# Kernel optimization log

Hardware: AMD Instinct MI355X
Metric: run time of the kernel (lower is better)

## Reference

```python
import jax, jax.numpy as jnp
import numpy as np
from jax import lax

EPS = 1e-5


def _conv1d(x, w, groups=1):
    # x: [B, Cin, L], w: [Cout, Cin/groups, K], padding=1, stride=1
    return lax.conv_general_dilated(
        x, w, window_strides=(1,), padding=[(1, 1)],
        dimension_numbers=('NCH', 'OIH', 'NCH'),
        feature_group_count=groups)


def _batchnorm(x, gamma, beta):
    # training-mode BatchNorm1d: stats over (batch, length), biased variance
    mean = jnp.mean(x, axis=(0, 2), keepdims=True)
    var = jnp.mean(jnp.square(x - mean), axis=(0, 2), keepdims=True)
    xn = (x - mean) * lax.rsqrt(var + EPS)
    return xn * gamma[None, :, None] + beta[None, :, None]


def setup_inputs() -> dict:
    key = jax.random.key(0)
    ks = jax.random.split(key, 8)
    B = 1 << 20  # 1,048,576
    x = jax.random.normal(ks[0], (B, 3), dtype=jnp.float32)
    # conv1: 1 -> 16, k=3 (xavier-normal-ish scale)
    w1 = jax.random.normal(ks[1], (16, 1, 3), dtype=jnp.float32) * 0.5
    b1 = jnp.zeros((16,), jnp.float32)
    g1 = jnp.ones((16,), jnp.float32)
    bt1 = jnp.zeros((16,), jnp.float32)
    # conv2: grouped, groups=16, 16 -> 32, k=3 -> weight [32, 1, 3]
    w2 = jax.random.normal(ks[2], (32, 1, 3), dtype=jnp.float32) * 0.5
    b2 = jnp.zeros((32,), jnp.float32)
    g2 = jnp.ones((32,), jnp.float32)
    bt2 = jnp.zeros((32,), jnp.float32)
    # fc1: Linear(32 -> 16) kaiming-normal-ish
    fw1 = jax.random.normal(ks[3], (16, 32), dtype=jnp.float32) * (2.0 / 32.0) ** 0.5
    fb1 = jnp.zeros((16,), jnp.float32)
    # fc2: Linear(16 -> 1); torch init sets these to 0, but use small random
    # values so gradients/outputs are non-degenerate for testing
    fw2 = jax.random.normal(ks[4], (1, 16), dtype=jnp.float32) * 0.1
    fb2 = jnp.zeros((1,), jnp.float32)
    return dict(x=x, w1=w1, b1=b1, g1=g1, bt1=bt1,
                w2=w2, b2=b2, g2=g2, bt2=bt2,
                fw1=fw1, fb1=fb1, fw2=fw2, fb2=fb2)


def reference(x, w1, b1, g1, bt1, w2, b2, g2, bt2, fw1, fb1, fw2, fb2):
    h = x[:, None, :]                                   # [B, 1, 3]
    h = _conv1d(h, w1) + b1[None, :, None]              # [B, 16, 3]
    h = _batchnorm(jax.nn.relu(h), g1, bt1)
    h = _conv1d(h, w2, groups=16) + b2[None, :, None]   # [B, 32, 3]
    h = _batchnorm(jax.nn.relu(h), g2, bt2)
    h = jnp.mean(h, axis=2)                             # AdaptiveAvgPool1d(1) -> [B, 32]
    h = jax.nn.relu(h @ fw1.T + fb1)                    # [B, 16]
    return h @ fw2.T + fb2                              # [B, 1]
```

## Files before the change

### kernel.cpp

```cpp
#include <hip/hip_runtime.h>
#include <math.h>

#define EPSV 1e-5f

__device__ __forceinline__ void conv3_relu(float x0, float x1, float x2,
                                           float wa, float wb, float wc, float bb,
                                           float& t0, float& t1, float& t2)
{
    t0 = fmaxf(fmaf(wb, x0, fmaf(wc, x1, bb)), 0.f);
    t1 = fmaxf(fmaf(wa, x0, fmaf(wb, x1, fmaf(wc, x2, bb))), 0.f);
    t2 = fmaxf(fmaf(wa, x1, fmaf(wb, x2, bb)), 0.f);
}

__global__ __launch_bounds__(256) void k_stats1(const float* __restrict__ x,
                                                const float* __restrict__ w1,
                                                const float* __restrict__ b1,
                                                float* __restrict__ partials,
                                                int B)
{
    __shared__ float4 sW1[16];
    int t = threadIdx.x;
    if (t < 16) sW1[t] = make_float4(w1[3*t], w1[3*t+1], w1[3*t+2], b1[t]);
    __syncthreads();

    float cur[32];
#pragma unroll
    for (int i = 0; i < 32; ++i) cur[i] = 0.f;

    auto upd = [&](int g, float t0, float t1, float t2) {
        cur[g]      += t0 + t1 + t2;
        cur[16 + g]  = fmaf(t0, t0, fmaf(t1, t1, fmaf(t2, t2, cur[16 + g])));
    };

    auto accum1 = [&](float x0, float x1, float x2) {
#pragma unroll
        for (int g = 0; g < 16; ++g) {
            float4 w = sW1[g];
            float t0, t1, t2;
            conv3_relu(x0, x1, x2, w.x, w.y, w.z, w.w, t0, t1, t2);
            upd(g, t0, t1, t2);
        }
    };

    int nchunk = (B + 3) >> 2;
    for (int ch = blockIdx.x * 256 + t; ch < nchunk; ch += gridDim.x * 256) {
        int s0 = ch << 2;
        if (s0 + 4 <= B) {
            const float4* xp = (const float4*)(x + (size_t)s0 * 3);
            float4 A = xp[0], Bq = xp[1], Cq = xp[2];
            const float xs[4][3] = {{A.x,  A.y,  A.z },
                                    {A.w,  Bq.x, Bq.y},
                                    {Bq.z, Bq.w, Cq.x},
                                    {Cq.y, Cq.z, Cq.w}};
#pragma unroll
            for (int g = 0; g < 16; ++g) {
                float4 w = sW1[g];
#pragma unroll
                for (int m = 0; m < 4; ++m) {
                    float t0, t1, t2;
                    conv3_relu(xs[m][0], xs[m][1], xs[m][2],
                               w.x, w.y, w.z, w.w, t0, t1, t2);
                    upd(g, t0, t1, t2);
                }
            }
        } else {
            for (int m = 0; m < 4; ++m) {
                int s = s0 + m;
                if (s < B) accum1(x[3*s], x[3*s+1], x[3*s+2]);
            }
        }
    }

    int lane = t & 63, wid = t >> 6;
#pragma unroll
    for (int i = 0; i < 32; ++i) cur[i] += __shfl_xor(cur[i], 32, 64);
#pragma unroll
    for (int half = 16; half >= 1; half >>= 1) {
#pragma unroll
        for (int i = 0; i < half; ++i) {
            bool up = (lane & half);
            float keep = up ? cur[i + half] : cur[i];
            float send = up ? cur[i] : cur[i + half];
            cur[i] = keep + __shfl_xor(send, half, 64);
        }
    }
    __shared__ float red[4][32];
    if (lane < 32) red[wid][lane] = cur[0];
    __syncthreads();
    if (t < 32)
        partials[blockIdx.x * 32 + t] = red[0][t] + red[1][t] + red[2][t] + red[3][t];
}

__global__ __launch_bounds__(256) void k_stats2(const float* __restrict__ x,
                                                const float* __restrict__ w1,
                                                const float* __restrict__ b1,
                                                const float* __restrict__ p1,
                                                const float* __restrict__ g1,
                                                const float* __restrict__ bt1,
                                                const float* __restrict__ w2,
                                                const float* __restrict__ b2,
                                                float* __restrict__ partials,
                                                float Ninv, int nb1, int B)
{
    __shared__ float4 sW1[16];
    __shared__ float4 sU[32];
    __shared__ float2 sC[32];
    __shared__ float4 redbuf[256];
    __shared__ float tot[32];
    __shared__ float ssc[16], ssh[16];
    int t = threadIdx.x;

    {
        int v4 = t & 7, c = t >> 3;
        float4 a = make_float4(0.f, 0.f, 0.f, 0.f);
        for (int b = c; b < nb1; b += 32) {
            float4 p = ((const float4*)p1)[b * 8 + v4];
            a.x += p.x; a.y += p.y; a.z += p.z; a.w += p.w;
        }
        redbuf[c * 8 + v4] = a;
    }
    if (t < 16) sW1[t] = make_float4(w1[3*t], w1[3*t+1], w1[3*t+2], b1[t]);
    __syncthreads();
    if (t < 8) {
        float4 a = make_float4(0.f, 0.f, 0.f, 0.f);
#pragma unroll
        for (int c = 0; c < 32; ++c) {
            float4 p = redbuf[c * 8 + t];
            a.x += p.x; a.y += p.y; a.z += p.z; a.w += p.w;
        }
        tot[4*t+0] = a.x; tot[4*t+1] = a.y; tot[4*t+2] = a.z; tot[4*t+3] = a.w;
    }
    __syncthreads();
    if (t < 16) {
        float mean = tot[t] * Ninv;
        float var  = fmaxf(tot[16 + t] * Ninv - mean * mean, 0.f);
        float rstd = rsqrtf(var + EPSV);
        float sc = g1[t] * rstd;
        ssc[t] = sc;
        ssh[t] = bt1[t] - mean * sc;
    }
    __syncthreads();
    if (t < 32) {
        int o = t, g = o >> 1;
        float sc = ssc[g], sh = ssh[g];
        float wv0 = w2[3*o], wv1 = w2[3*o+1], wv2 = w2[3*o+2];
        sU[o] = make_float4(wv0 * sc, wv1 * sc, wv2 * sc,
                            b2[o] + sh * (wv1 + wv2));
        sC[o] = make_float2(b2[o] + sh * (wv0 + wv1 + wv2),
                            b2[o] + sh * (wv0 + wv1));
    }
    __syncthreads();

    const int p = t & 1;
    const int gbase = 8 * p;

    float cur[32];
#pragma unroll
    for (int i = 0; i < 32; ++i) cur[i] = 0.f;

    auto updc = [&](int oc, float v0, float v1, float v2) {
        cur[oc]      += v0 + v1 + v2;
        cur[16 + oc]  = fmaf(v0, v0, fmaf(v1, v1, fmaf(v2, v2, cur[16 + oc])));
    };

    auto accum4 = [&](const float4& A, const float4& Bq, const float4& Cq) {
        const float xs[4][3] = {{A.x,  A.y,  A.z },
                                {A.w,  Bq.x, Bq.y},
                                {Bq.z, Bq.w, Cq.x},
                                {Cq.y, Cq.z, Cq.w}};
#pragma unroll
        for (int g = 0; g < 8; ++g) {
            float4 w = sW1[gbase + g];
            float r[4][3];
#pragma unroll
            for (int m = 0; m < 4; ++m)
                conv3_relu(xs[m][0], xs[m][1], xs[m][2],
                           w.x, w.y, w.z, w.w, r[m][0], r[m][1], r[m][2]);
#pragma unroll
            for (int jj = 0; jj < 2; ++jj) {
                int oc = 2 * g + jj;
                int oo = 16 * p + oc;
                float4 u = sU[oo];
                float2 cc = sC[oo];
#pragma unroll
                for (int m = 0; m < 4; ++m) {
                    float v0 = fmaxf(fmaf(u.y, r[m][0], fmaf(u.z, r[m][1], u.w)), 0.f);
                    float v1 = fmaxf(fmaf(u.x, r[m][0], fmaf(u.y, r[m][1], fmaf(u.z, r[m][2], cc.x))), 0.f);
                    float v2 = fmaxf(fmaf(u.x, r[m][1], fmaf(u.y, r[m][2], cc.y)), 0.f);
                    updc(oc, v0, v1, v2);
                }
            }
        }
    };

    auto accum1 = [&](float x0, float x1, float x2) {
#pragma unroll
        for (int g = 0; g < 8; ++g) {
            float4 w = sW1[gbase + g];
            float r0, r1, r2;
            conv3_relu(x0, x1, x2, w.x, w.y, w.z, w.w, r0, r1, r2);
#pragma unroll
            for (int jj = 0; jj < 2; ++jj) {
                int oc = 2 * g + jj;
                int oo = 16 * p + oc;
                float4 u = sU[oo];
                float2 cc = sC[oo];
                float v0 = fmaxf(fmaf(u.y, r0, fmaf(u.z, r1, u.w)), 0.f);
                float v1 = fmaxf(fmaf(u.x, r0, fmaf(u.y, r1, fmaf(u.z, r2, cc.x))), 0.f);
                float v2 = fmaxf(fmaf(u.x, r1, fmaf(u.y, r2, cc.y)), 0.f);
                updc(oc, v0, v1, v2);
            }
        }
    };

    int nchunk = (B + 3) >> 2;
    int gp     = (blockIdx.x * 256 + t) >> 1;
    int stride = (gridDim.x * 256) >> 1;
    for (int ch = gp; ch < nchunk; ch += stride) {
        int s0 = ch << 2;
        if (s0 + 4 <= B) {
            const float4* xp = (const float4*)(x + (size_t)s0 * 3);
            float4 A = xp[0], Bq = xp[1], Cq = xp[2];
            accum4(A, Bq, Cq);
        } else {
            for (int m = 0; m < 4; ++m) {
                int s = s0 + m;
                if (s < B) accum1(x[3*s], x[3*s+1], x[3*s+2]);
            }
        }
    }

    int lane = t & 63, wid = t >> 6;
#pragma unroll
    for (int half = 16; half >= 1; half >>= 1) {
        int d = half << 1;
#pragma unroll
        for (int i = 0; i < half; ++i) {
            bool up = (lane & d);
            float keep = up ? cur[i + half] : cur[i];
            float send = up ? cur[i] : cur[i + half];
            cur[i] = keep + __shfl_xor(send, d, 64);
        }
    }
    __shared__ float red[4][64];
    {
        int idx = lane >> 1;
        int v = ((idx >> 4) << 5) + 16 * p + (idx & 15);
        red[wid][v] = cur[0];
    }
    __syncthreads();
    if (t < 64)
        partials[blockIdx.x * 64 + t] = red[0][t] + red[1][t] + red[2][t] + red[3][t];
}

__global__ __launch_bounds__(256, 2) void k_final(const float* __restrict__ x,
                                                  const float* __restrict__ w1,
                                                  const float* __restrict__ b1,
                                                  const float* __restrict__ w2,
                                                  const float* __restrict__ b2,
                                                  const float* __restrict__ g1,
                                                  const float* __restrict__ bt1,
                                                  const float* __restrict__ g2,
                                                  const float* __restrict__ bt2,
                                                  const float* __restrict__ fw1,
                                                  const float* __restrict__ fb1,
                                                  const float* __restrict__ fw2,
                                                  const float* __restrict__ fb2,
                                                  const float* __restrict__ p1,
                                                  const float* __restrict__ p2,
                                                  float* __restrict__ out,
                                                  float Ninv, int nb1, int nb2, int B)
{
    __shared__ float4 sW1[16];
    __shared__ float4 sU[32];
    __shared__ float2 sC[32];
    __shared__ float4 sFT[128];
    __shared__ float2 sJ[16];
    __shared__ float  sb2;
    __shared__ float4 redbuf[256];
    __shared__ float tot1[32];
    __shared__ float tot2[64];
    __shared__ float ssc1[16], ssh1[16];
    __shared__ float ssc2[32], ssh2[32];
    int t = threadIdx.x;

    {
        int v4 = t & 7, c = t >> 3;
        float4 a = make_float4(0.f, 0.f, 0.f, 0.f);
        for (int b = c; b < nb1; b += 32) {
            float4 p = ((const float4*)p1)[b * 8 + v4];
            a.x += p.x; a.y += p.y; a.z += p.z; a.w += p.w;
        }
        redbuf[c * 8 + v4] = a;
    }
    if (t < 16) sW1[t] = make_float4(w1[3*t], w1[3*t+1], w1[3*t+2], b1[t]);
    if (t == 224) sb2 = fb2[0];
    __syncthreads();
    if (t < 8) {
        float4 a = make_float4(0.f, 0.f, 0.f, 0.f);
#pragma unroll
        for (int c = 0; c < 32; ++c) {
            float4 p = redbuf[c * 8 + t];
            a.x += p.x; a.y += p.y; a.z += p.z; a.w += p.w;
        }
        tot1[4*t+0] = a.x; tot1[4*t+1] = a.y; tot1[4*t+2] = a.z; tot1[4*t+3] = a.w;
    }
    __syncthreads();
    if (t < 16) {
        float mean = tot1[t] * Ninv;
        float var  = fmaxf(tot1[16 + t] * Ninv - mean * mean, 0.f);
        float rstd = rsqrtf(var + EPSV);
        float sc = g1[t] * rstd;
        ssc1[t] = sc;
        ssh1[t] = bt1[t] - mean * sc;
    }
    __syncthreads();
    if (t < 32) {
        int o = t, g = o >> 1;
        float sc = ssc1[g], sh = ssh1[g];
        float wv0 = w2[3*o], wv1 = w2[3*o+1], wv2 = w2[3*o+2];
        sU[o] = make_float4(wv0 * sc, wv1 * sc, wv2 * sc,
                            b2[o] + sh * (wv1 + wv2));
        sC[o] = make_float2(b2[o] + sh * (wv0 + wv1 + wv2),
                            b2[o] + sh * (wv0 + wv1));
    }
    {
        int v4 = t & 15, c = t >> 4;
        float4 a = make_float4(0.f, 0.f, 0.f, 0.f);
        for (int b = c; b < nb2; b += 16) {
            float4 p = ((const float4*)p2)[b * 16 + v4];
            a.x += p.x; a.y += p.y; a.z += p.z; a.w += p.w;
        }
        redbuf[c * 16 + v4] = a;
    }
    __syncthreads();
    if (t < 16) {
        float4 a = make_float4(0.f, 0.f, 0.f, 0.f);
#pragma unroll
        for (int c = 0; c < 16; ++c) {
            float4 p = redbuf[c * 16 + t];
            a.x += p.x; a.y += p.y; a.z += p.z; a.w += p.w;
        }
        tot2[4*t+0] = a.x; tot2[4*t+1] = a.y; tot2[4*t+2] = a.z; tot2[4*t+3] = a.w;
    }
    __syncthreads();
    if (t < 32) {
        float mean = tot2[t] * Ninv;
        float var  = fmaxf(tot2[32 + t] * Ninv - mean * mean, 0.f);
        float rstd = rsqrtf(var + EPSV);
        float sc = g2[t] * rstd;
        ssc2[t] = sc;
        ssh2[t] = bt2[t] - mean * sc;
    }
    __syncthreads();
    for (int idx = t; idx < 512; idx += 256) {
        int o = idx >> 4, j = idx & 15;
        ((float*)sFT)[o * 16 + j] = fw1[j * 32 + o] * ssc2[o] * (1.0f / 3.0f);
    }
    if (t < 16) {
        float a = fb1[t];
#pragma unroll
        for (int c = 0; c < 32; ++c) a = fmaf(fw1[t * 32 + c], ssh2[c], a);
        sJ[t] = make_float2(a, fw2[t]);
    }
    __syncthreads();

    int nchunk = (B + 3) >> 2;
    for (int ch = blockIdx.x * 256 + t; ch < nchunk; ch += gridDim.x * 256) {
        int s0 = ch << 2;
        if (s0 + 4 <= B) {
            const float4* xp = (const float4*)(x + (size_t)s0 * 3);
            float4 A = xp[0], Bq = xp[1], Cq = xp[2];
            const float xs[4][3] = {{A.x,  A.y,  A.z },
                                    {A.w,  Bq.x, Bq.y},
                                    {Bq.z, Bq.w, Cq.x},
                                    {Cq.y, Cq.z, Cq.w}};

            float acc[4][16];
#pragma unroll
            for (int m = 0; m < 4; ++m)
#pragma unroll
                for (int j = 0; j < 16; ++j) acc[m][j] = 0.f;

#pragma unroll 4
            for (int g = 0; g < 16; ++g) {
                float4 w = sW1[g];
                float r[4][3];
#pragma unroll
                for (int m = 0; m < 4; ++m)
                    conv3_relu(xs[m][0], xs[m][1], xs[m][2],
                               w.x, w.y, w.z, w.w, r[m][0], r[m][1], r[m][2]);
#pragma unroll
                for (int jj = 0; jj < 2; ++jj) {
                    int o = 2 * g + jj;
                    float4 u = sU[o];
                    float2 cc = sC[o];
                    float so[4];
#pragma unroll
                    for (int m = 0; m < 4; ++m) {
                        float v0 = fmaxf(fmaf(u.y, r[m][0], fmaf(u.z, r[m][1], u.w)), 0.f);
                        float v1 = fmaxf(fmaf(u.x, r[m][0], fmaf(u.y, r[m][1], fmaf(u.z, r[m][2], cc.x))), 0.f);
                        float v2 = fmaxf(fmaf(u.x, r[m][1], fmaf(u.y, r[m][2], cc.y)), 0.f);
                        so[m] = v0 + v1 + v2;
                    }
#pragma unroll
                    for (int k = 0; k < 4; ++k) {
                        float4 f = sFT[o * 4 + k];
#pragma unroll
                        for (int m = 0; m < 4; ++m) {
                            acc[m][4*k+0] = fmaf(f.x, so[m], acc[m][4*k+0]);
                            acc[m][4*k+1] = fmaf(f.y, so[m], acc[m][4*k+1]);
                            acc[m][4*k+2] = fmaf(f.z, so[m], acc[m][4*k+2]);
                            acc[m][4*k+3] = fmaf(f.w, so[m], acc[m][4*k+3]);
                        }
                    }
                }
            }

            float res[4];
#pragma unroll
            for (int m = 0; m < 4; ++m) res[m] = sb2;
#pragma unroll
            for (int j = 0; j < 16; ++j) {
                float2 jw = sJ[j];
#pragma unroll
                for (int m = 0; m < 4; ++m)
                    res[m] = fmaf(jw.y, fmaxf(acc[m][j] + jw.x, 0.f), res[m]);
            }
            *(float4*)(out + s0) = make_float4(res[0], res[1], res[2], res[3]);
        } else {
            for (int m = 0; m < 4; ++m) {
                int s = s0 + m;
                if (s >= B) break;
                float x0 = x[3*s], x1 = x[3*s+1], x2 = x[3*s+2];
                float acc1[16];
#pragma unroll
                for (int j = 0; j < 16; ++j) acc1[j] = 0.f;
#pragma unroll 4
                for (int g = 0; g < 16; ++g) {
                    float4 w = sW1[g];
                    float r0, r1, r2;
                    conv3_relu(x0, x1, x2, w.x, w.y, w.z, w.w, r0, r1, r2);
#pragma unroll
                    for (int jj = 0; jj < 2; ++jj) {
                        int o = 2 * g + jj;
                        float4 u = sU[o];
                        float2 cc = sC[o];
                        float v0 = fmaxf(fmaf(u.y, r0, fmaf(u.z, r1, u.w)), 0.f);
                        float v1 = fmaxf(fmaf(u.x, r0, fmaf(u.y, r1, fmaf(u.z, r2, cc.x))), 0.f);
                        float v2 = fmaxf(fmaf(u.x, r1, fmaf(u.y, r2, cc.y)), 0.f);
                        float so = v0 + v1 + v2;
#pragma unroll
                        for (int k = 0; k < 4; ++k) {
                            float4 f = sFT[o * 4 + k];
                            acc1[4*k+0] = fmaf(f.x, so, acc1[4*k+0]);
                            acc1[4*k+1] = fmaf(f.y, so, acc1[4*k+1]);
                            acc1[4*k+2] = fmaf(f.z, so, acc1[4*k+2]);
                            acc1[4*k+3] = fmaf(f.w, so, acc1[4*k+3]);
                        }
                    }
                }
                float r = sb2;
#pragma unroll
                for (int j = 0; j < 16; ++j) {
                    float2 jw = sJ[j];
                    r = fmaf(jw.y, fmaxf(acc1[j] + jw.x, 0.f), r);
                }
                out[s] = r;
            }
        }
    }
}

extern "C" void kernel_launch(void* const* d_in, const int* in_sizes, int n_in,
                              void* d_out, int out_size, void* d_ws, size_t ws_size,
                              hipStream_t stream)
{
    const float* x   = (const float*)d_in[0];
    const float* w1  = (const float*)d_in[1];
    const float* b1  = (const float*)d_in[2];
    const float* g1  = (const float*)d_in[3];
    const float* bt1 = (const float*)d_in[4];
    const float* w2  = (const float*)d_in[5];
    const float* b2  = (const float*)d_in[6];
    const float* g2  = (const float*)d_in[7];
    const float* bt2 = (const float*)d_in[8];
    const float* fw1 = (const float*)d_in[9];
    const float* fb1 = (const float*)d_in[10];
    const float* fw2 = (const float*)d_in[11];
    const float* fb2 = (const float*)d_in[12];

    int B = in_sizes[0] / 3;

    int nb1 = 512;
    int nb2 = 512;
    while ((size_t)(nb1 * 32 + nb2 * 64) * sizeof(float) > ws_size && nb1 > 1) {
        nb1 >>= 1; nb2 >>= 1;
    }

    float* ws = (float*)d_ws;
    float* p1 = ws;
    float* p2 = ws + (size_t)nb1 * 32;

    float Ninv = 1.0f / (3.0f * (float)B);

    int nchunk = (B + 3) / 4;
    int gridF = (nchunk + 255) / 256;
    if (gridF > 2048) gridF = 2048;

    k_stats1<<<nb1, 256, 0, stream>>>(x, w1, b1, p1, B);
    k_stats2<<<nb2, 256, 0, stream>>>(x, w1, b1, p1, g1, bt1, w2, b2,
                                      p2, Ninv, nb1, B);
    k_final<<<gridF, 256, 0, stream>>>(x, w1, b1, w2, b2, g1, bt1, g2, bt2,
                                       fw1, fb1, fw2, fb2, p1, p2,
                                       (float*)d_out, Ninv, nb1, nb2, B);
}
```

Baseline: 164.5 us.

## Fuse three passes into one persistent kernel with software grid barriers

Replaces the three separate kernels (stats1, stats2, final) with one persistent kernel. It runs the three phases in sequence, separated by atomic-counter grid barriers, and sizes the grid from occupancy capped at 512 blocks. The aim is to remove kernel launch gaps and to let each block reuse its shared-memory setup. In exchange the final phase runs on at most 512 blocks instead of up to 2048, and every barrier adds spin-wait latency. The barrier relies on all blocks being co-resident and adds a memset launch per call.

```diff
diff --git a/kernel.cpp b/kernel.cpp
--- a/kernel.cpp
+++ b/kernel.cpp
@@ -12,264 +12,41 @@
     t2 = fmaxf(fmaf(wa, x1, fmaf(wb, x2, bb)), 0.f);
 }
 
-__global__ __launch_bounds__(256) void k_stats1(const float* __restrict__ x,
-                                                const float* __restrict__ w1,
-                                                const float* __restrict__ b1,
-                                                float* __restrict__ partials,
-                                                int B)
+__device__ __forceinline__ void grid_barrier(int* count, int* gen, int nb)
 {
-    __shared__ float4 sW1[16];
-    int t = threadIdx.x;
-    if (t < 16) sW1[t] = make_float4(w1[3*t], w1[3*t+1], w1[3*t+2], b1[t]);
     __syncthreads();
-
-    float cur[32];
-#pragma unroll
-    for (int i = 0; i < 32; ++i) cur[i] = 0.f;
-
-    auto upd = [&](int g, float t0, float t1, float t2) {
-        cur[g]      += t0 + t1 + t2;
-        cur[16 + g]  = fmaf(t0, t0, fmaf(t1, t1, fmaf(t2, t2, cur[16 + g])));
-    };
-
-    auto accum1 = [&](float x0, float x1, float x2) {
-#pragma unroll
-        for (int g = 0; g < 16; ++g) {
-            float4 w = sW1[g];
-            float t0, t1, t2;
-            conv3_relu(x0, x1, x2, w.x, w.y, w.z, w.w, t0, t1, t2);
-            upd(g, t0, t1, t2);
-        }
-    };
-
-    int nchunk = (B + 3) >> 2;
-    for (int ch = blockIdx.x * 256 + t; ch < nchunk; ch += gridDim.x * 256) {
-        int s0 = ch << 2;
-        if (s0 + 4 <= B) {
-            const float4* xp = (const float4*)(x + (size_t)s0 * 3);
-            float4 A = xp[0], Bq = xp[1], Cq = xp[2];
-            const float xs[4][3] = {{A.x,  A.y,  A.z },
-                                    {A.w,  Bq.x, Bq.y},
-                                    {Bq.z, Bq.w, Cq.x},
-                                    {Cq.y, Cq.z, Cq.w}};
-#pragma unroll
-            for (int g = 0; g < 16; ++g) {
-                float4 w = sW1[g];
-#pragma unroll
-                for (int m = 0; m < 4; ++m) {
-                    float t0, t1, t2;
-                    conv3_relu(xs[m][0], xs[m][1], xs[m][2],
-                               w.x, w.y, w.z, w.w, t0, t1, t2);
-                    upd(g, t0, t1, t2);
-                }
-            }
+    if (threadIdx.x == 0) {
+        __threadfence();
+        int g = atomicAdd(gen, 0);
+        if (atomicAdd(count, 1) == nb - 1) {
+            atomicExch(count, 0);
+            atomicAdd(gen, 1);
         } else {
-            for (int m = 0; m < 4; ++m) {
-                int s = s0 + m;
-                if (s < B) accum1(x[3*s], x[3*s+1], x[3*s+2]);
-            }
-        }
-    }
-
-    int lane = t & 63, wid = t >> 6;
-#pragma unroll
-    for (int i = 0; i < 32; ++i) cur[i] += __shfl_xor(cur[i], 32, 64);
-#pragma unroll
-    for (int half = 16; half >= 1; half >>= 1) {
-#pragma unroll
-        for (int i = 0; i < half; ++i) {
-            bool up = (lane & half);
-            float keep = up ? cur[i + half] : cur[i];
-            float send = up ? cur[i] : cur[i + half];
-            cur[i] = keep + __shfl_xor(send, half, 64);
-        }
-    }
-    __shared__ float red[4][32];
-    if (lane < 32) red[wid][lane] = cur[0];
-    __syncthreads();
-    if (t < 32)
-        partials[blockIdx.x * 32 + t] = red[0][t] + red[1][t] + red[2][t] + red[3][t];
-}
-
-__global__ __launch_bounds__(256) void k_stats2(const float* __restrict__ x,
-                                                const float* __restrict__ w1,
-                                                const float* __restrict__ b1,
-                                                const float* __restrict__ p1,
-                                                const float* __restrict__ g1,
-                                                const float* __restrict__ bt1,
-                                                const float* __restrict__ w2,
-                                                const float* __restrict__ b2,
-                                                float* __restrict__ partials,
-                                                float Ninv, int nb1, int B)
-{
-    __shared__ float4 sW1[16];
-    __shared__ float4 sU[32];
-    __shared__ float2 sC[32];
-    __shared__ float4 redbuf[256];
-    __shared__ float tot[32];
-    __shared__ float ssc[16], ssh[16];
-    int t = threadIdx.x;
-
-    {
-        int v4 = t & 7, c = t >> 3;
-        float4 a = make_float4(0.f, 0.f, 0.f, 0.f);
-        for (int b = c; b < nb1; b += 32) {
-            float4 p = ((const float4*)p1)[b * 8 + v4];
-            a.x += p.x; a.y += p.y; a.z += p.z; a.w += p.w;
-        }
-        redbuf[c * 8 + v4] = a;
-    }
-    if (t < 16) sW1[t] = make_float4(w1[3*t], w1[3*t+1], w1[3*t+2], b1[t]);
-    __syncthreads();
-    if (t < 8) {
-        float4 a = make_float4(0.f, 0.f, 0.f, 0.f);
-#pragma unroll
-        for (int c = 0; c < 32; ++c) {
-            float4 p = redbuf[c * 8 + t];
-            a.x += p.x; a.y += p.y; a.z += p.z; a.w += p.w;
-        }
-        tot[4*t+0] = a.x; tot[4*t+1] = a.y; tot[4*t+2] = a.z; tot[4*t+3] = a.w;
+            while (atomicAdd(gen, 0) == g) __builtin_amdgcn_s_sleep(2);
+        }
+        __threadfence();
     }
     __syncthreads();
-    if (t < 16) {
-        float mean = tot[t] * Ninv;
-        float var  = fmaxf(tot[16 + t] * Ninv - mean * mean, 0.f);
-        float rstd = rsqrtf(var + EPSV);
-        float sc = g1[t] * rstd;
-        ssc[t] = sc;
-        ssh[t] = bt1[t] - mean * sc;
-    }
-    __syncthreads();
-    if (t < 32) {
-        int o = t, g = o >> 1;
-        float sc = ssc[g], sh = ssh[g];
-        float wv0 = w2[3*o], wv1 = w2[3*o+1], wv2 = w2[3*o+2];
-        sU[o] = make_float4(wv0 * sc, wv1 * sc, wv2 * sc,
-                            b2[o] + sh * (wv1 + wv2));
-        sC[o] = make_float2(b2[o] + sh * (wv0 + wv1 + wv2),
-                            b2[o] + sh * (wv0 + wv1));
-    }
-    __syncthreads();
-
-    const int p = t & 1;
-    const int gbase = 8 * p;
-
-    float cur[32];
-#pragma unroll
-    for (int i = 0; i < 32; ++i) cur[i] = 0.f;
-
-    auto updc = [&](int oc, float v0, float v1, float v2) {
-        cur[oc]      += v0 + v1 + v2;
-        cur[16 + oc]  = fmaf(v0, v0, fmaf(v1, v1, fmaf(v2, v2, cur[16 + oc])));
-    };
-
-    auto accum4 = [&](const float4& A, const float4& Bq, const float4& Cq) {
-        const float xs[4][3] = {{A.x,  A.y,  A.z },
-                                {A.w,  Bq.x, Bq.y},
-                                {Bq.z, Bq.w, Cq.x},
-                                {Cq.y, Cq.z, Cq.w}};
-#pragma unroll
-        for (int g = 0; g < 8; ++g) {
-            float4 w = sW1[gbase + g];
-            float r[4][3];
-#pragma unroll
-            for (int m = 0; m < 4; ++m)
-                conv3_relu(xs[m][0], xs[m][1], xs[m][2],
-                           w.x, w.y, w.z, w.w, r[m][0], r[m][1], r[m][2]);
-#pragma unroll
-            for (int jj = 0; jj < 2; ++jj) {
-                int oc = 2 * g + jj;
-                int oo = 16 * p + oc;
-                float4 u = sU[oo];
-                float2 cc = sC[oo];
-#pragma unroll
-                for (int m = 0; m < 4; ++m) {
-                    float v0 = fmaxf(fmaf(u.y, r[m][0], fmaf(u.z, r[m][1], u.w)), 0.f);
-                    float v1 = fmaxf(fmaf(u.x, r[m][0], fmaf(u.y, r[m][1], fmaf(u.z, r[m][2], cc.x))), 0.f);
-                    float v2 = fmaxf(fmaf(u.x, r[m][1], fmaf(u.y, r[m][2], cc.y)), 0.f);
-                    updc(oc, v0, v1, v2);
-                }
-            }
-        }
-    };
-
-    auto accum1 = [&](float x0, float x1, float x2) {
-#pragma unroll
-        for (int g = 0; g < 8; ++g) {
-            float4 w = sW1[gbase + g];
-            float r0, r1, r2;
-            conv3_relu(x0, x1, x2, w.x, w.y, w.z, w.w, r0, r1, r2);
-#pragma unroll
-            for (int jj = 0; jj < 2; ++jj) {
-                int oc = 2 * g + jj;
-                int oo = 16 * p + oc;
-                float4 u = sU[oo];
-                float2 cc = sC[oo];
-                float v0 = fmaxf(fmaf(u.y, r0, fmaf(u.z, r1, u.w)), 0.f);
-                float v1 = fmaxf(fmaf(u.x, r0, fmaf(u.y, r1, fmaf(u.z, r2, cc.x))), 0.f);
-                float v2 = fmaxf(fmaf(u.x, r1, fmaf(u.y, r2, cc.y)), 0.f);
-                updc(oc, v0, v1, v2);
-            }
-        }
-    };
-
-    int nchunk = (B + 3) >> 2;
-    int gp     = (blockIdx.x * 256 + t) >> 1;
-    int stride = (gridDim.x * 256) >> 1;
-    for (int ch = gp; ch < nchunk; ch += stride) {
-        int s0 = ch << 2;
-        if (s0 + 4 <= B) {
-            const float4* xp = (const float4*)(x + (size_t)s0 * 3);
-            float4 A = xp[0], Bq = xp[1], Cq = xp[2];
-            accum4(A, Bq, Cq);
-        } else {
-            for (int m = 0; m < 4; ++m) {
-                int s = s0 + m;
-                if (s < B) accum1(x[3*s], x[3*s+1], x[3*s+2]);
-            }
-        }
-    }
-
-    int lane = t & 63, wid = t >> 6;
-#pragma unroll
-    for (int half = 16; half >= 1; half >>= 1) {
-        int d = half << 1;
-#pragma unroll
-        for (int i = 0; i < half; ++i) {
-            bool up = (lane & d);
-            float keep = up ? cur[i + half] : cur[i];
-            float send = up ? cur[i] : cur[i + half];
-            cur[i] = keep + __shfl_xor(send, d, 64);
-        }
-    }
-    __shared__ float red[4][64];
-    {
-        int idx = lane >> 1;
-        int v = ((idx >> 4) << 5) + 16 * p + (idx & 15);
-        red[wid][v] = cur[0];
-    }
-    __syncthreads();
-    if (t < 64)
-        partials[blockIdx.x * 64 + t] = red[0][t] + red[1][t] + red[2][t] + red[3][t];
 }
 
-__global__ __launch_bounds__(256, 2) void k_final(const float* __restrict__ x,
-                                                  const float* __restrict__ w1,
-                                                  const float* __restrict__ b1,
-                                                  const float* __restrict__ w2,
-                                                  const float* __restrict__ b2,
-                                                  const float* __restrict__ g1,
-                                                  const float* __restrict__ bt1,
-                                                  const float* __restrict__ g2,
-                                                  const float* __restrict__ bt2,
-                                                  const float* __restrict__ fw1,
-                                                  const float* __restrict__ fb1,
-                                                  const float* __restrict__ fw2,
-                                                  const float* __restrict__ fb2,
-                                                  const float* __restrict__ p1,
-                                                  const float* __restrict__ p2,
-                                                  float* __restrict__ out,
-                                                  float Ninv, int nb1, int nb2, int B)
+__global__ __launch_bounds__(256) void k_fused(const float* __restrict__ x,
+                                               const float* __restrict__ w1,
+                                               const float* __restrict__ b1,
+                                               const float* __restrict__ g1,
+                                               const float* __restrict__ bt1,
+                                               const float* __restrict__ w2,
+                                               const float* __restrict__ b2,
+                                               const float* __restrict__ g2,
+                                               const float* __restrict__ bt2,
+                                               const float* __restrict__ fw1,
+                                               const float* __restrict__ fb1,
+                                               const float* __restrict__ fw2,
+                                               const float* __restrict__ fb2,
+                                               float* __restrict__ p1,
+                                               float* __restrict__ p2,
+                                               int* __restrict__ bar,
+                                               float* __restrict__ out,
+                                               float Ninv, int B)
 {
     __shared__ float4 sW1[16];
     __shared__ float4 sU[32];
@@ -278,113 +55,146 @@
     __shared__ float2 sJ[16];
     __shared__ float  sb2;
     __shared__ float4 redbuf[256];
-    __shared__ float tot1[32];
-    __shared__ float tot2[64];
-    __shared__ float ssc1[16], ssh1[16];
-    __shared__ float ssc2[32], ssh2[32];
+    __shared__ float  tot[64];
+    __shared__ float  ssc[32], ssh[32];
+    __shared__ float  sRed[4][64];
+
     int t = threadIdx.x;
+    int nchunk = (B + 3) >> 2;
+    int NBg = gridDim.x;
 
     {
-        int v4 = t & 7, c = t >> 3;
-        float4 a = make_float4(0.f, 0.f, 0.f, 0.f);
-        for (int b = c; b < nb1; b += 32) {
-            float4 p = ((const float4*)p1)[b * 8 + v4];
-            a.x += p.x; a.y += p.y; a.z += p.z; a.w += p.w;
-        }
-        redbuf[c * 8 + v4] = a;
+        if (t < 16) sW1[t] = make_float4(w1[3*t], w1[3*t+1], w1[3*t+2], b1[t]);
+        __syncthreads();
+
+        float cur[32];
+#pragma unroll
+        for (int i = 0; i < 32; ++i) cur[i] = 0.f;
+
+        auto upd = [&](int g, float t0, float t1, float t2) {
+            cur[g]      += t0 + t1 + t2;
+            cur[16 + g]  = fmaf(t0, t0, fmaf(t1, t1, fmaf(t2, t2, cur[16 + g])));
+        };
+
+        auto accum1 = [&](float x0, float x1, float x2) {
+#pragma unroll
+            for (int g = 0; g < 16; ++g) {
+                float4 w = sW1[g];
+                float t0, t1, t2;
+                conv3_relu(x0, x1, x2, w.x, w.y, w.z, w.w, t0, t1, t2);
+                upd(g, t0, t1, t2);
+            }
+        };
+
+        for (int ch = blockIdx.x * 256 + t; ch < nchunk; ch += NBg * 256) {
+            int s0 = ch << 2;
+            if (s0 + 4 <= B) {
+                const float4* xp = (const float4*)(x + (size_t)s0 * 3);
+                float4 A = xp[0], Bq = xp[1], Cq = xp[2];
+                const float xs[4][3] = {{A.x,  A.y,  A.z },
+                                        {A.w,  Bq.x, Bq.y},
+                                        {Bq.z, Bq.w, Cq.x},
+                                        {Cq.y, Cq.z, Cq.w}};
+#pragma unroll
+                for (int g = 0; g < 16; ++g) {
+                    float4 w = sW1[g];
+#pragma unroll
+                    for (int m = 0; m < 4; ++m) {
+                        float t0, t1, t2;
+                        conv3_relu(xs[m][0], xs[m][1], xs[m][2],
+                                   w.x, w.y, w.z, w.w, t0, t1, t2);
+                        upd(g, t0, t1, t2);
+                    }
+                }
+            } else {
+                for (int m = 0; m < 4; ++m) {
+                    int s = s0 + m;
+                    if (s < B) accum1(x[3*s], x[3*s+1], x[3*s+2]);
+                }
+            }
+        }
+
+        int lane = t & 63, wid = t >> 6;
+#pragma unroll
+        for (int i = 0; i < 32; ++i) cur[i] += __shfl_xor(cur[i], 32, 64);
+#pragma unroll
+        for (int half = 16; half >= 1; half >>= 1) {
+#pragma unroll
+            for (int i = 0; i < half; ++i) {
+                bool up = (lane & half);
+                float keep = up ? cur[i + half] : cur[i];
+                float send = up ? cur[i] : cur[i + half];
+                cur[i] = keep + __shfl_xor(send, half, 64);
+            }
+        }
+        if (lane < 32) sRed[wid][lane] = cur[0];
+        __syncthreads();
+        if (t < 32)
+            p1[blockIdx.x * 32 + t] = sRed[0][t] + sRed[1][t] + sRed[2][t] + sRed[3][t];
     }
-    if (t < 16) sW1[t] = make_float4(w1[3*t], w1[3*t+1], w1[3*t+2], b1[t]);
-    if (t == 224) sb2 = fb2[0];
-    __syncthreads();
-    if (t < 8) {
-        float4 a = make_float4(0.f, 0.f, 0.f, 0.f);
-#pragma unroll
-        for (int c = 0; c < 32; ++c) {
-            float4 p = redbuf[c * 8 + t];
-            a.x += p.x; a.y += p.y; a.z += p.z; a.w += p.w;
-        }
-        tot1[4*t+0] = a.x; tot1[4*t+1] = a.y; tot1[4*t+2] = a.z; tot1[4*t+3] = a.w;
-    }
-    __syncthreads();
-    if (t < 16) {
-        float mean = tot1[t] * Ninv;
-        float var  = fmaxf(tot1[16 + t] * Ninv - mean * mean, 0.f);
-        float rstd = rsqrtf(var + EPSV);
-        float sc = g1[t] * rstd;
-        ssc1[t] = sc;
-        ssh1[t] = bt1[t] - mean * sc;
-    }
-    __syncthreads();
-    if (t < 32) {
-        int o = t, g = o >> 1;
-        float sc = ssc1[g], sh = ssh1[g];
-        float wv0 = w2[3*o], wv1 = w2[3*o+1], wv2 = w2[3*o+2];
-        sU[o] = make_float4(wv0 * sc, wv1 * sc, wv2 * sc,
-                            b2[o] + sh * (wv1 + wv2));
-        sC[o] = make_float2(b2[o] + sh * (wv0 + wv1 + wv2),
-                            b2[o] + sh * (wv0 + wv1));
-    }
+    grid_barrier(bar, bar + 1, NBg);
+
     {
-        int v4 = t & 15, c = t >> 4;
-        float4 a = make_float4(0.f, 0.f, 0.f, 0.f);
-        for (int b = c; b < nb2; b += 16) {
-            float4 p = ((const float4*)p2)[b * 16 + v4];
-            a.x += p.x; a.y += p.y; a.z += p.z; a.w += p.w;
-        }
-        redbuf[c * 16 + v4] = a;
-    }
-    __syncthreads();
-    if (t < 16) {
-        float4 a = make_float4(0.f, 0.f, 0.f, 0.f);
-#pragma unroll
-        for (int c = 0; c < 16; ++c) {
-            float4 p = redbuf[c * 16 + t];
-            a.x += p.x; a.y += p.y; a.z += p.z; a.w += p.w;
-        }
-        tot2[4*t+0] = a.x; tot2[4*t+1] = a.y; tot2[4*t+2] = a.z; tot2[4*t+3] = a.w;
-    }
-    __syncthreads();
-    if (t < 32) {
-        float mean = tot2[t] * Ninv;
-        float var  = fmaxf(tot2[32 + t] * Ninv - mean * mean, 0.f);
-        float rstd = rsqrtf(var + EPSV);
-        float sc = g2[t] * rstd;
-        ssc2[t] = sc;
-        ssh2[t] = bt2[t] - mean * sc;
-    }
-    __syncthreads();
-    for (int idx = t; idx < 512; idx += 256) {
-        int o = idx >> 4, j = idx & 15;
-        ((float*)sFT)[o * 16 + j] = fw1[j * 32 + o] * ssc2[o] * (1.0f / 3.0f);
-    }
-    if (t < 16) {
-        float a = fb1[t];
-#pragma unroll
-        for (int c = 0; c < 32; ++c) a = fmaf(fw1[t * 32 + c], ssh2[c], a);
-        sJ[t] = make_float2(a, fw2[t]);
-    }
-    __syncthreads();
-
-    int nchunk = (B + 3) >> 2;
-    for (int ch = blockIdx.x * 256 + t; ch < nchunk; ch += gridDim.x * 256) {
-        int s0 = ch << 2;
-        if (s0 + 4 <= B) {
-            const float4* xp = (const float4*)(x + (size_t)s0 * 3);
-            float4 A = xp[0], Bq = xp[1], Cq = xp[2];
+        {
+            int v4 = t & 7, c = t >> 3;
+            float4 a = make_float4(0.f, 0.f, 0.f, 0.f);
+            for (int b = c; b < NBg; b += 32) {
+                float4 p = ((const float4*)p1)[b * 8 + v4];
+                a.x += p.x; a.y += p.y; a.z += p.z; a.w += p.w;
+            }
+            redbuf[c * 8 + v4] = a;
+        }
+        __syncthreads();
+        if (t < 8) {
+            float4 a = make_float4(0.f, 0.f, 0.f, 0.f);
+#pragma unroll
+            for (int c = 0; c < 32; ++c) {
+                float4 p = redbuf[c * 8 + t];
+                a.x += p.x; a.y += p.y; a.z += p.z; a.w += p.w;
+            }
+            tot[4*t+0] = a.x; tot[4*t+1] = a.y; tot[4*t+2] = a.z; tot[4*t+3] = a.w;
+        }
+        __syncthreads();
+        if (t < 16) {
+            float mean = tot[t] * Ninv;
+            float var  = fmaxf(tot[16 + t] * Ninv - mean * mean, 0.f);
+            float rstd = rsqrtf(var + EPSV);
+            float sc = g1[t] * rstd;
+            ssc[t] = sc;
+            ssh[t] = bt1[t] - mean * sc;
+        }
+        __syncthreads();
+        if (t < 32) {
+            int o = t, g = o >> 1;
+            float sc = ssc[g], sh = ssh[g];
+            float wv0 = w2[3*o], wv1 = w2[3*o+1], wv2 = w2[3*o+2];
+            sU[o] = make_float4(wv0 * sc, wv1 * sc, wv2 * sc,
+                                b2[o] + sh * (wv1 + wv2));
+            sC[o] = make_float2(b2[o] + sh * (wv0 + wv1 + wv2),
+                                b2[o] + sh * (wv0 + wv1));
+        }
+        __syncthreads();
+
+        const int p = t & 1;
+        const int gbase = 8 * p;
+
+        float cur[32];
+#pragma unroll
+        for (int i = 0; i < 32; ++i) cur[i] = 0.f;
+
+        auto updc = [&](int oc, float v0, float v1, float v2) {
+            cur[oc]      += v0 + v1 + v2;
+            cur[16 + oc]  = fmaf(v0, v0, fmaf(v1, v1, fmaf(v2, v2, cur[16 + oc])));
+        };
+
+        auto accum4 = [&](const float4& A, const float4& Bq, const float4& Cq) {
             const float xs[4][3] = {{A.x,  A.y,  A.z },
                                     {A.w,  Bq.x, Bq.y},
                                     {Bq.z, Bq.w, Cq.x},
                                     {Cq.y, Cq.z, Cq.w}};
-
-            float acc[4][16];
-#pragma unroll
-            for (int m = 0; m < 4; ++m)
-#pragma unroll
-                for (int j = 0; j < 16; ++j) acc[m][j] = 0.f;
-
-#pragma unroll 4
-            for (int g = 0; g < 16; ++g) {
-                float4 w = sW1[g];
+#pragma unroll
+            for (int g = 0; g < 8; ++g) {
+                float4 w = sW1[gbase + g];
                 float r[4][3];
 #pragma unroll
                 for (int m = 0; m < 4; ++m)
@@ -392,81 +202,225 @@
                                w.x, w.y, w.z, w.w, r[m][0], r[m][1], r[m][2]);
 #pragma unroll
                 for (int jj = 0; jj < 2; ++jj) {
-                    int o = 2 * g + jj;
-                    float4 u = sU[o];
-                    float2 cc = sC[o];
-                    float so[4];
+                    int oc = 2 * g + jj;
+                    int oo = 16 * p + oc;
+                    float4 u = sU[oo];
+                    float2 cc = sC[oo];
 #pragma unroll
                     for (int m = 0; m < 4; ++m) {
                         float v0 = fmaxf(fmaf(u.y, r[m][0], fmaf(u.z, r[m][1], u.w)), 0.f);
                         float v1 = fmaxf(fmaf(u.x, r[m][0], fmaf(u.y, r[m][1], fmaf(u.z, r[m][2], cc.x))), 0.f);
                         float v2 = fmaxf(fmaf(u.x, r[m][1], fmaf(u.y, r[m][2], cc.y)), 0.f);
-                        so[m] = v0 + v1 + v2;
+                        updc(oc, v0, v1, v2);
                     }
-#pragma unroll
-                    for (int k = 0; k < 4; ++k) {
-                        float4 f = sFT[o * 4 + k];
-#pragma unroll
-                        for (int m = 0; m < 4; ++m) {
-                            acc[m][4*k+0] = fmaf(f.x, so[m], acc[m][4*k+0]);
-                            acc[m][4*k+1] = fmaf(f.y, so[m], acc[m][4*k+1]);
-                            acc[m][4*k+2] = fmaf(f.z, so[m], acc[m][4*k+2]);
-                            acc[m][4*k+3] = fmaf(f.w, so[m], acc[m][4*k+3]);
-                        }
-                    }
-                }
-            }
-
-            float res[4];
-#pragma unroll
-            for (int m = 0; m < 4; ++m) res[m] = sb2;
-#pragma unroll
-            for (int j = 0; j < 16; ++j) {
-                float2 jw = sJ[j];
+                }
+            }
+        };
+
+        auto accum1 = [&](float x0, float x1, float x2) {
+#pragma unroll
+            for (int g = 0; g < 8; ++g) {
+                float4 w = sW1[gbase + g];
+                float r0, r1, r2;
+                conv3_relu(x0, x1, x2, w.x, w.y, w.z, w.w, r0, r1, r2);
+#pragma unroll
+                for (int jj = 0; jj < 2; ++jj) {
+                    int oc = 2 * g + jj;
+                    int oo = 16 * p + oc;
+                    float4 u = sU[oo];
+                    float2 cc = sC[oo];
+                    float v0 = fmaxf(fmaf(u.y, r0, fmaf(u.z, r1, u.w)), 0.f);
+                    float v1 = fmaxf(fmaf(u.x, r0, fmaf(u.y, r1, fmaf(u.z, r2, cc.x))), 0.f);
+                    float v2 = fmaxf(fmaf(u.x, r1, fmaf(u.y, r2, cc.y)), 0.f);
+                    updc(oc, v0, v1, v2);
+                }
+            }
+        };
+
+        int gp     = (blockIdx.x * 256 + t) >> 1;
+        int stride = (NBg * 256) >> 1;
+        for (int ch = gp; ch < nchunk; ch += stride) {
+            int s0 = ch << 2;
+            if (s0 + 4 <= B) {
+                const float4* xp = (const float4*)(x + (size_t)s0 * 3);
+                float4 A = xp[0], Bq = xp[1], Cq = xp[2];
+                accum4(A, Bq, Cq);
+            } else {
+                for (int m = 0; m < 4; ++m) {
+                    int s = s0 + m;
+                    if (s < B) accum1(x[3*s], x[3*s+1], x[3*s+2]);
+                }
+            }
+        }
+
+        int lane = t & 63, wid = t >> 6;
+#pragma unroll
+        for (int half = 16; half >= 1; half >>= 1) {
+            int d = half << 1;
+#pragma unroll
+            for (int i = 0; i < half; ++i) {
+                bool up = (lane & d);
+                float keep = up ? cur[i + half] : cur[i];
+                float send = up ? cur[i] : cur[i + half];
+                cur[i] = keep + __shfl_xor(send, d, 64);
+            }
+        }
+        {
+            int idx = lane >> 1;
+            int v = ((idx >> 4) << 5) + 16 * p + (idx & 15);
+            sRed[wid][v] = cur[0];
+        }
+        __syncthreads();
+        if (t < 64)
+            p2[blockIdx.x * 64 + t] = sRed[0][t] + sRed[1][t] + sRed[2][t] + sRed[3][t];
+    }
+    grid_barrier(bar, bar + 1, NBg);
+
+    {
+        {
+            int v4 = t & 15, c = t >> 4;
+            float4 a = make_float4(0.f, 0.f, 0.f, 0.f);
+            for (int b = c; b < NBg; b += 16) {
+                float4 p = ((const float4*)p2)[b * 16 + v4];
+                a.x += p.x; a.y += p.y; a.z += p.z; a.w += p.w;
+            }
+            redbuf[c * 16 + v4] = a;
+        }
+        if (t == 224) sb2 = fb2[0];
+        __syncthreads();
+        if (t < 16) {
+            float4 a = make_float4(0.f, 0.f, 0.f, 0.f);
+#pragma unroll
+            for (int c = 0; c < 16; ++c) {
+                float4 p = redbuf[c * 16 + t];
+                a.x += p.x; a.y += p.y; a.z += p.z; a.w += p.w;
+            }
+            tot[4*t+0] = a.x; tot[4*t+1] = a.y; tot[4*t+2] = a.z; tot[4*t+3] = a.w;
+        }
+        __syncthreads();
+        if (t < 32) {
+            float mean = tot[t] * Ninv;
+            float var  = fmaxf(tot[32 + t] * Ninv - mean * mean, 0.f);
+            float rstd = rsqrtf(var + EPSV);
+            float sc = g2[t] * rstd;
+            ssc[t] = sc;
+            ssh[t] = bt2[t] - mean * sc;
+        }
+        __syncthreads();
+        for (int idx = t; idx < 512; idx += 256) {
+            int o = idx >> 4, j = idx & 15;
+            ((float*)sFT)[o * 16 + j] = fw1[j * 32 + o] * ssc[o] * (1.0f / 3.0f);
+        }
+        if (t < 16) {
+            float a = fb1[t];
+#pragma unroll
+            for (int c = 0; c < 32; ++c) a = fmaf(fw1[t * 32 + c], ssh[c], a);
+            sJ[t] = make_float2(a, fw2[t]);
+        }
+        __syncthreads();
+
+        for (int ch = blockIdx.x * 256 + t; ch < nchunk; ch += NBg * 256) {
+            int s0 = ch << 2;
+            if (s0 + 4 <= B) {
+                const float4* xp = (const float4*)(x + (size_t)s0 * 3);
+                float4 A = xp[0], Bq = xp[1], Cq = xp[2];
+                const float xs[4][3] = {{A.x,  A.y,  A.z },
+                                        {A.w,  Bq.x, Bq.y},
+                                        {Bq.z, Bq.w, Cq.x},
+                                        {Cq.y, Cq.z, Cq.w}};
+
+                float acc[4][16];
 #pragma unroll
                 for (int m = 0; m < 4; ++m)
-                    res[m] = fmaf(jw.y, fmaxf(acc[m][j] + jw.x, 0.f), res[m]);
-            }
-            *(float4*)(out + s0) = make_float4(res[0], res[1], res[2], res[3]);
-        } else {
-            for (int m = 0; m < 4; ++m) {
-                int s = s0 + m;
-                if (s >= B) break;
-                float x0 = x[3*s], x1 = x[3*s+1], x2 = x[3*s+2];
-                float acc1[16];
-#pragma unroll
-                for (int j = 0; j < 16; ++j) acc1[j] = 0.f;
+#pragma unroll
+                    for (int j = 0; j < 16; ++j) acc[m][j] = 0.f;
+
 #pragma unroll 4
                 for (int g = 0; g < 16; ++g) {
                     float4 w = sW1[g];
-                    float r0, r1, r2;
-                    conv3_relu(x0, x1, x2, w.x, w.y, w.z, w.w, r0, r1, r2);
+                    float r[4][3];
+#pragma unroll
+                    for (int m = 0; m < 4; ++m)
+                        conv3_relu(xs[m][0], xs[m][1], xs[m][2],
+                                   w.x, w.y, w.z, w.w, r[m][0], r[m][1], r[m][2]);
 #pragma unroll
                     for (int jj = 0; jj < 2; ++jj) {
                         int o = 2 * g + jj;
                         float4 u = sU[o];
                         float2 cc = sC[o];
-                        float v0 = fmaxf(fmaf(u.y, r0, fmaf(u.z, r1, u.w)), 0.f);
-                        float v1 = fmaxf(fmaf(u.x, r0, fmaf(u.y, r1, fmaf(u.z, r2, cc.x))), 0.f);
-                        float v2 = fmaxf(fmaf(u.x, r1, fmaf(u.y, r2, cc.y)), 0.f);
-                        float so = v0 + v1 + v2;
+                        float so[4];
+#pragma unroll
+                        for (int m = 0; m < 4; ++m) {
+                            float v0 = fmaxf(fmaf(u.y, r[m][0], fmaf(u.z, r[m][1], u.w)), 0.f);
+                            float v1 = fmaxf(fmaf(u.x, r[m][0], fmaf(u.y, r[m][1], fmaf(u.z, r[m][2], cc.x))), 0.f);
+                            float v2 = fmaxf(fmaf(u.x, r[m][1], fmaf(u.y, r[m][2], cc.y)), 0.f);
+                            so[m] = v0 + v1 + v2;
+                        }
 #pragma unroll
                         for (int k = 0; k < 4; ++k) {
                             float4 f = sFT[o * 4 + k];
-                            acc1[4*k+0] = fmaf(f.x, so, acc1[4*k+0]);
-                            acc1[4*k+1] = fmaf(f.y, so, acc1[4*k+1]);
-                            acc1[4*k+2] = fmaf(f.z, so, acc1[4*k+2]);
-                            acc1[4*k+3] = fmaf(f.w, so, acc1[4*k+3]);
+#pragma unroll
+                            for (int m = 0; m < 4; ++m) {
+                                acc[m][4*k+0] = fmaf(f.x, so[m], acc[m][4*k+0]);
+                                acc[m][4*k+1] = fmaf(f.y, so[m], acc[m][4*k+1]);
+                                acc[m][4*k+2] = fmaf(f.z, so[m], acc[m][4*k+2]);
+                                acc[m][4*k+3] = fmaf(f.w, so[m], acc[m][4*k+3]);
+                            }
                         }
                     }
                 }
-                float r = sb2;
+
+                float res[4];
+#pragma unroll
+                for (int m = 0; m < 4; ++m) res[m] = sb2;
 #pragma unroll
                 for (int j = 0; j < 16; ++j) {
                     float2 jw = sJ[j];
-                    r = fmaf(jw.y, fmaxf(acc1[j] + jw.x, 0.f), r);
-                }
-                out[s] = r;
+#pragma unroll
+                    for (int m = 0; m < 4; ++m)
+                        res[m] = fmaf(jw.y, fmaxf(acc[m][j] + jw.x, 0.f), res[m]);
+                }
+                *(float4*)(out + s0) = make_float4(res[0], res[1], res[2], res[3]);
+            } else {
+                for (int m = 0; m < 4; ++m) {
+                    int s = s0 + m;
+                    if (s >= B) break;
+                    float x0 = x[3*s], x1 = x[3*s+1], x2 = x[3*s+2];
+                    float acc1[16];
+#pragma unroll
+                    for (int j = 0; j < 16; ++j) acc1[j] = 0.f;
+#pragma unroll 4
+                    for (int g = 0; g < 16; ++g) {
+                        float4 w = sW1[g];
+                        float r0, r1, r2;
+                        conv3_relu(x0, x1, x2, w.x, w.y, w.z, w.w, r0, r1, r2);
+#pragma unroll
+                        for (int jj = 0; jj < 2; ++jj) {
+                            int o = 2 * g + jj;
+                            float4 u = sU[o];
+                            float2 cc = sC[o];
+                            float v0 = fmaxf(fmaf(u.y, r0, fmaf(u.z, r1, u.w)), 0.f);
+                            float v1 = fmaxf(fmaf(u.x, r0, fmaf(u.y, r1, fmaf(u.z, r2, cc.x))), 0.f);
+                            float v2 = fmaxf(fmaf(u.x, r1, fmaf(u.y, r2, cc.y)), 0.f);
+                            float so = v0 + v1 + v2;
+#pragma unroll
+                            for (int k = 0; k < 4; ++k) {
+                                float4 f = sFT[o * 4 + k];
+                                acc1[4*k+0] = fmaf(f.x, so, acc1[4*k+0]);
+                                acc1[4*k+1] = fmaf(f.y, so, acc1[4*k+1]);
+                                acc1[4*k+2] = fmaf(f.z, so, acc1[4*k+2]);
+                                acc1[4*k+3] = fmaf(f.w, so, acc1[4*k+3]);
+                            }
+                        }
+                    }
+                    float r = sb2;
+#pragma unroll
+                    for (int j = 0; j < 16; ++j) {
+                        float2 jw = sJ[j];
+                        r = fmaf(jw.y, fmaxf(acc1[j] + jw.x, 0.f), r);
+                    }
+                    out[s] = r;
+                }
             }
         }
     }
@@ -492,26 +446,29 @@
 
     int B = in_sizes[0] / 3;
 
-    int nb1 = 512;
-    int nb2 = 512;
-    while ((size_t)(nb1 * 32 + nb2 * 64) * sizeof(float) > ws_size && nb1 > 1) {
-        nb1 >>= 1; nb2 >>= 1;
+    static int gridN = 0;
+    if (gridN == 0) {
+        int perCU = 0;
+        hipOccupancyMaxActiveBlocksPerMultiprocessor(&perCU, k_fused, 256, 0);
+        if (perCU < 1) perCU = 1;
+        long cap = (long)perCU * 256;
+        gridN = (cap < 512) ? (int)cap : 512;
+        if (gridN < 1) gridN = 256;
     }
-
-    float* ws = (float*)d_ws;
-    float* p1 = ws;
-    float* p2 = ws + (size_t)nb1 * 32;
+    int NB = gridN;
+    while ((size_t)(NB * 96 + 2) * sizeof(float) > ws_size && NB > 1) NB >>= 1;
+
+    float* ws  = (float*)d_ws;
+    float* p1  = ws;
+    float* p2  = ws + (size_t)NB * 32;
+    int*   bar = (int*)(p2 + (size_t)NB * 64);
+    float* outp = (float*)d_out;
 
     float Ninv = 1.0f / (3.0f * (float)B);
 
-    int nchunk = (B + 3) / 4;
-    int gridF = (nchunk + 255) / 256;
-    if (gridF > 2048) gridF = 2048;
-
-    k_stats1<<<nb1, 256, 0, stream>>>(x, w1, b1, p1, B);
-    k_stats2<<<nb2, 256, 0, stream>>>(x, w1, b1, p1, g1, bt1, w2, b2,
-                                      p2, Ninv, nb1, B);
-    k_final<<<gridF, 256, 0, stream>>>(x, w1, b1, w2, b2, g1, bt1, g2, bt2,
-                                       fw1, fb1, fw2, fb2, p1, p2,
-                                       (float*)d_out, Ninv, nb1, nb2, B);
+    hipMemsetAsync(bar, 0, 2 * sizeof(int), stream);
+
+    k_fused<<<NB, 256, 0, stream>>>(x, w1, b1, g1, bt1, w2, b2, g2, bt2,
+                                    fw1, fb1, fw2, fb2, p1, p2, bar,
+                                    outp, Ninv, B);
 }
```

New measurement: 187.7 us. 14.1% more time.
